# Kernel optimization log

Measured on AMD Instinct MI355X. Metric: run time of the kernel, lower is better.

## Reference

```python
import jax, jax.numpy as jnp
import numpy as np

RPN_BBOX_STD_DEV = np.array([0.1, 0.1, 0.2, 0.2], dtype=np.float32)
PRE_NMS_LIMIT = 6000
PROPOSAL_COUNT = 1000
NMS_THRESHOLD = 0.7
BATCH = 8
NUM_ANCHORS = 261888


def setup_inputs() -> dict:
    key = jax.random.key(0)
    k1, k2, k3, k4 = jax.random.split(key, 4)
    fg = jax.random.uniform(k1, (BATCH, NUM_ANCHORS), dtype=jnp.float32)
    rpn_probs = jnp.stack([1.0 - fg, fg], axis=-1)  # [B, N, 2] (bg, fg)
    rpn_bbox = jax.random.normal(k2, (BATCH, NUM_ANCHORS, 4), dtype=jnp.float32) * 0.5
    # valid normalized anchors: y_min < y_max, x_min < x_max, inside [0, 1]
    mins = jax.random.uniform(k3, (BATCH, NUM_ANCHORS, 2), minval=0.0, maxval=0.85)
    size = jax.random.uniform(k4, (BATCH, NUM_ANCHORS, 2), minval=0.02, maxval=0.15)
    anchors = jnp.concatenate([mins, mins + size], axis=-1)  # [B, N, 4]
    return {"rpn_probs": rpn_probs, "rpn_bbox": rpn_bbox, "anchors": anchors}


def apply_box_deltas(boxes, deltas):
    # boxes: [..., (y1, x1, y2, x2)], deltas: [..., (dy, dx, log(dh), log(dw))]
    h = boxes[..., 2] - boxes[..., 0]
    w = boxes[..., 3] - boxes[..., 1]
    cy = boxes[..., 0] + 0.5 * h + deltas[..., 0] * h
    cx = boxes[..., 1] + 0.5 * w + deltas[..., 1] * w
    h = h * jnp.exp(deltas[..., 2])
    w = w * jnp.exp(deltas[..., 3])
    y1 = cy - 0.5 * h
    x1 = cx - 0.5 * w
    return jnp.stack([y1, x1, y1 + h, x1 + w], axis=-1)


def pairwise_iou(boxes):
    # boxes: [N, 4] -> iou [N, N]
    y1, x1, y2, x2 = boxes[:, 0], boxes[:, 1], boxes[:, 2], boxes[:, 3]
    area = (y2 - y1) * (x2 - x1)
    ih = jnp.maximum(jnp.minimum(y2[:, None], y2[None, :]) - jnp.maximum(y1[:, None], y1[None, :]), 0.0)
    iw = jnp.maximum(jnp.minimum(x2[:, None], x2[None, :]) - jnp.maximum(x1[:, None], x1[None, :]), 0.0)
    inter = ih * iw
    union = area[:, None] + area[None, :] - inter
    return jnp.where(union > 0.0, inter / union, 0.0)


def nms_single(boxes):
    # boxes: [K, 4], already sorted by score descending (top_k sorted=True).
    # Greedy NMS: a box is suppressed if it overlaps (IoU > thresh) a kept,
    # higher-scoring box. Sequential suppression via lax.scan over rows.
    K = boxes.shape[0]
    iou = pairwise_iou(boxes)  # [K, K]
    order = jnp.arange(K)

    def step(keep, i):
        suppress = keep[i] & (iou[i] > NMS_THRESHOLD) & (order > i)
        return keep & ~suppress, None

    keep, _ = jax.lax.scan(step, jnp.ones((K,), dtype=bool), order)
    # gather kept boxes in score order, pad with zeros to PROPOSAL_COUNT
    rank = jnp.cumsum(keep) - 1
    valid = keep & (rank < PROPOSAL_COUNT)
    dest = jnp.where(valid, rank, PROPOSAL_COUNT)  # invalid rows -> scratch row
    out = jnp.zeros((PROPOSAL_COUNT + 1, 4), boxes.dtype).at[dest].set(boxes)
    return out[:PROPOSAL_COUNT]


def reference(rpn_probs, rpn_bbox, anchors):
    scores = rpn_probs[:, :, 1]  # fg prob [B, N]
    deltas = rpn_bbox * jnp.asarray(RPN_BBOX_STD_DEV).reshape(1, 1, 4)
    k = min(PRE_NMS_LIMIT, anchors.shape[1])
    top_scores, idx = jax.lax.top_k(scores, k)  # sorted descending, [B, K]
    deltas_k = jnp.take_along_axis(deltas, idx[..., None], axis=1)   # [B, K, 4]
    anchors_k = jnp.take_along_axis(anchors, idx[..., None], axis=1)  # [B, K, 4]
    boxes = jnp.clip(apply_box_deltas(anchors_k, deltas_k), 0.0, 1.0)
    proposals = jax.vmap(nms_single)(boxes)  # [B, PROPOSAL_COUNT, 4]
    return proposals
```

## Files before the change

kernel.cpp:

```cpp
#include <hip/hip_runtime.h>
#include <hip/hip_bf16.h>

typedef unsigned long long ull;

constexpr int BATCH = 8;
constexpr int NA    = 261888;
constexpr int KSEL  = 6000;
constexpr int PROP  = 1000;
constexpr int CAP   = 8192;
constexpr int NBINS = 8192;
constexpr int HB    = 16;
constexpr int NB    = (KSEL + 63) / 64;
constexpr int NWP   = 94;
constexpr int NBLK  = 94;
constexpr int NBLK2 = 47;

constexpr size_t OFF_CNT   = 0;
constexpr size_t OFF_TSEL  = 512;
constexpr size_t OFF_BOXES = 544;
constexpr size_t OFF_MASK  = 769024;
constexpr size_t OFF_DIAG  = OFF_MASK + 36096000;
constexpr size_t OFF_SUP   = OFF_DIAG + 385024;
constexpr size_t OFF_KEYS  = OFF_MASK;
constexpr size_t OFF_RANK  = OFF_MASK + 524288;
constexpr size_t OFF_HIST  = OFF_MASK + 2097152;

__device__ __forceinline__ int score_bin(float s) {
  int b = (int)(s * (float)NBINS);
  if (b < 0) b = 0;
  if (b > NBINS - 1) b = NBINS - 1;
  return b;
}

__global__ __launch_bounds__(256) void hist_kernel(const float2* __restrict__ probs,
                                                   unsigned int* __restrict__ hist) {
  __shared__ unsigned int lh[NBINS];
  for (int i = threadIdx.x; i < NBINS; i += 256) lh[i] = 0u;
  __syncthreads();
  int b = blockIdx.y;
  const float2* p = probs + (size_t)b * NA;
  for (int a = blockIdx.x * 256 + threadIdx.x; a < NA; a += HB * 256) {
    atomicAdd(&lh[score_bin(p[a].y)], 1u);
  }
  __syncthreads();
  unsigned int* gh = hist + ((size_t)b * HB + blockIdx.x) * NBINS;
  for (int i = threadIdx.x; i < NBINS; i += 256) gh[i] = lh[i];
}

__global__ __launch_bounds__(256) void thresh_kernel(const unsigned int* __restrict__ hist,
                                                     int* __restrict__ tsel) {
  constexpr int GR = NBINS / 256;
  __shared__ unsigned int ch[NBINS];
  __shared__ unsigned int gsum[256];
  int b = blockIdx.x;
  const unsigned int* h = hist + (size_t)b * HB * NBINS;
  for (int bin = threadIdx.x; bin < NBINS; bin += 256) {
    unsigned int s = 0;
    for (int k = 0; k < HB; ++k) s += h[(size_t)k * NBINS + bin];
    ch[bin] = s;
  }
  __syncthreads();
  unsigned int s = 0;
  int g0 = threadIdx.x * GR;
  for (int i = 0; i < GR; ++i) s += ch[g0 + i];
  gsum[threadIdx.x] = s;
  __syncthreads();
  if (threadIdx.x == 0) {
    unsigned int acc = 0;
    int g = 255;
    for (; g > 0; --g) {
      if (acc + gsum[g] >= (unsigned)KSEL) break;
      acc += gsum[g];
    }
    int t = g * GR;
    for (int bin = g * GR + GR - 1; bin >= g * GR; --bin) {
      acc += ch[bin];
      if (acc >= (unsigned)KSEL) { t = bin; break; }
    }
    tsel[b] = t;
  }
}

__global__ __launch_bounds__(256) void compact_kernel(const float2* __restrict__ probs,
                                                      const int* __restrict__ tsel,
                                                      int* __restrict__ cnt,
                                                      ull* __restrict__ keys) {
  __shared__ int lcnt, lbase;
  __shared__ ull lbuf[2048];
  int b = blockIdx.y;
  int t = tsel[b];
  if (threadIdx.x == 0) lcnt = 0;
  __syncthreads();
  const float2* p = probs + (size_t)b * NA;
  for (int a = blockIdx.x * blockDim.x + threadIdx.x; a < NA; a += gridDim.x * blockDim.x) {
    float s = p[a].y;
    if (score_bin(s) >= t) {
      int pos = atomicAdd(&lcnt, 1);
      unsigned int ib = ~__float_as_uint(s);
      lbuf[pos] = ((ull)ib << 32) | (unsigned int)a;
    }
  }
  __syncthreads();
  if (threadIdx.x == 0) lbase = atomicAdd(&cnt[b * 16], lcnt);
  __syncthreads();
  int n = lcnt, base = lbase;
  ull* kb = keys + (size_t)b * CAP;
  for (int i = threadIdx.x; i < n; i += 256) {
    int pos = base + i;
    if (pos < CAP) kb[pos] = lbuf[i];
  }
}

__global__ __launch_bounds__(256) void rank_kernel(const int* __restrict__ cnt,
                                                   const ull* __restrict__ keys,
                                                   unsigned int* __restrict__ rank) {
  int b = blockIdx.z;
  int n = cnt[b * 16];
  if (n > CAP) n = CAP;
  int i = blockIdx.x * 256 + threadIdx.x;
  if (i >= n) return;
  const ull* kb = keys + (size_t)b * CAP;
  ull my = kb[i];
  int n16 = (n + 15) & ~15;
  int nchunks = n16 >> 4;
  int hc = nchunks >> 1;
  int jlo = (blockIdx.y == 0) ? 0 : hc * 16;
  int jhi = (blockIdx.y == 0) ? hc * 16 : n16;
  unsigned int r = 0;
  for (int j = jlo; j < jhi; j += 16) {
#pragma unroll
    for (int t = 0; t < 16; ++t) {
      r += (kb[j + t] < my) ? 1u : 0u;
    }
  }
  if (r) atomicAdd(&rank[(size_t)b * CAP + i], r);
}

__global__ __launch_bounds__(256) void scatter_kernel(const float4* __restrict__ anchors4,
                                                      const float4* __restrict__ bbox4,
                                                      const int* __restrict__ cnt,
                                                      const ull* __restrict__ keys,
                                                      const unsigned int* __restrict__ rank,
                                                      float4* __restrict__ boxes4) {
#pragma clang fp contract(off)
  int b = blockIdx.y;
  int n = cnt[b * 16];
  if (n > CAP) n = CAP;
  int i = blockIdx.x * 256 + threadIdx.x;
  if (i >= n) return;
  unsigned int r = rank[(size_t)b * CAP + i];
  if (r >= (unsigned)KSEL) return;
  int a = (int)(unsigned int)(keys[(size_t)b * CAP + i] & 0xffffffffull);
  float4 anc = anchors4[(size_t)b * NA + a];
  float4 d   = bbox4[(size_t)b * NA + a];
  float h = anc.z - anc.x;
  float w = anc.w - anc.y;
  float dy = d.x * 0.1f, dx = d.y * 0.1f, dh = d.z * 0.2f, dw = d.w * 0.2f;
  float cy = (anc.x + (0.5f * h)) + (dy * h);
  float cx = (anc.y + (0.5f * w)) + (dx * w);
  float h2 = h * expf(dh);
  float w2 = w * expf(dw);
  float y1 = cy - 0.5f * h2;
  float x1 = cx - 0.5f * w2;
  float y2 = y1 + h2;
  float x2 = x1 + w2;
  y1 = fminf(fmaxf(y1, 0.f), 1.f);
  x1 = fminf(fmaxf(x1, 0.f), 1.f);
  y2 = fminf(fmaxf(y2, 0.f), 1.f);
  x2 = fminf(fmaxf(x2, 0.f), 1.f);
  boxes4[(size_t)b * KSEL + r] = make_float4(y1, x1, y2, x2);
}

__global__ __launch_bounds__(256) void mask_kernel(const float4* __restrict__ boxes4,
                                                   ull* __restrict__ mask,
                                                   ull* __restrict__ diagT,
                                                   ull* __restrict__ superT) {
  int cx = blockIdx.x, rb2 = blockIdx.y, b = blockIdx.z;
  int w0 = 2 * rb2;
  int cb0 = w0 + 4 * cx;
  if (cb0 >= NWP) return;
  __shared__ float4 colbox[4][64];
  __shared__ float  colca[4][64];
  __shared__ ull wtile[128][5];
  int tid = threadIdx.x, wv = tid >> 6, l = tid & 63;
  int cb = cb0 + wv;
  int rA = rb2 * 128 + l, rB = rA + 64;
  float4 zero = make_float4(0.f, 0.f, 0.f, 0.f);
  float4 boxA = (rA < KSEL) ? boxes4[(size_t)b * KSEL + rA] : zero;
  float4 boxB = (rB < KSEL) ? boxes4[(size_t)b * KSEL + rB] : zero;
  float areaA = (boxA.z - boxA.x) * (boxA.w - boxA.y);
  float areaB = (boxB.z - boxB.x) * (boxB.w - boxB.y);
  int c = cb * 64 + l;
  float4 cload = (cb < NB && c < KSEL) ? boxes4[(size_t)b * KSEL + c] : zero;
  colbox[wv][l] = cload;
  colca[wv][l] = (cload.z - cload.x) * (cload.w - cload.y);
  __syncthreads();
  ull bitsA = 0ull, bitsB = 0ull;
  if (cb < NB) {
#pragma unroll
    for (int u = 0; u < 64; ++u) {
      float4 cbx = colbox[wv][u];
      float ca = colca[wv][u];
      {
        float ih = fmaxf(fminf(boxA.z, cbx.z) - fmaxf(boxA.x, cbx.x), 0.f);
        float iw = fmaxf(fminf(boxA.w, cbx.w) - fmaxf(boxA.y, cbx.y), 0.f);
        float inter = ih * iw;
        float uni = (areaA + ca) - inter;
        float d = fmaf(-0.7f, uni, inter);
        float tt = 6e-7f * uni;
        bool keep;
        if (__builtin_fabsf(d) <= tt) keep = (inter / uni) > 0.7f;
        else keep = d > 0.f;
        if (keep) bitsA |= (1ull << u);
      }
      {
        float ih = fmaxf(fminf(boxB.z, cbx.z) - fmaxf(boxB.x, cbx.x), 0.f);
        float iw = fmaxf(fminf(boxB.w, cbx.w) - fmaxf(boxB.y, cbx.y), 0.f);
        float inter = ih * iw;
        float uni = (areaB + ca) - inter;
        float d = fmaf(-0.7f, uni, inter);
        float tt = 6e-7f * uni;
        bool keep;
        if (__builtin_fabsf(d) <= tt) keep = (inter / uni) > 0.7f;
        else keep = d > 0.f;
        if (keep) bitsB |= (1ull << u);
      }
    }
    if (cb == w0) {
      bitsA &= (l == 63) ? 0ull : (~0ull << (l + 1));
      diagT[((size_t)b * NBLK + w0) * 64 + l] = bitsA;
    }
    if (cb == w0 + 1) {
      superT[((size_t)b * NBLK + w0) * 64 + l] = bitsA;
      bitsB &= (l == 63) ? 0ull : (~0ull << (l + 1));
      diagT[((size_t)b * NBLK + w0 + 1) * 64 + l] = bitsB;
    }
    if (cb == w0 + 2) {
      superT[((size_t)b * NBLK + w0 + 1) * 64 + l] = bitsB;
    }
  }
  wtile[l][wv] = bitsA;
  wtile[l + 64][wv] = bitsB;
  __syncthreads();
  int base_row = rb2 * 128;
#pragma unroll
  for (int pass = 0; pass < 2; ++pass) {
    int idx = pass * 256 + tid;
    int rr = idx >> 2, w = idx & 3;
    int row = base_row + rr;
    if (row < KSEL && cb0 + w < NWP)
      mask[((size_t)b * KSEL + row) * NWP + cb0 + w] = wtile[rr][w];
  }
}

__global__ __launch_bounds__(64) void transq_kernel(ull* __restrict__ diagT) {
  __shared__ ull rows[64];
  int n = blockIdx.x, b = blockIdx.y;
  int l = threadIdx.x;
  ull* base = diagT + ((size_t)b * NBLK + n) * 64;
  rows[l] = base[l];
  __syncthreads();
  ull col = 0ull;
#pragma unroll
  for (int r = 0; r < 64; ++r)
    col |= ((rows[r] >> l) & 1ull) << r;
  base[l] = col;
}

__global__ __launch_bounds__(256, 1) void scan_kernel(const float4* __restrict__ boxes4,
                                                      const ull* __restrict__ mask,
                                                      const ull* __restrict__ diagT,
                                                      const ull* __restrict__ superT,
                                                      float4* __restrict__ out4) {
  __shared__ ull ldiagT[NBLK * 64];
  __shared__ ull lsuper[NBLK * 64];
  __shared__ ull S[96];
  __shared__ ull S_urg;
  __shared__ int klist[2][64];
  __shared__ int skeep[1024];
  __shared__ int s_kept, s_done, s_klen[2];
  int b = blockIdx.x;
  int tid = threadIdx.x;
  int lane = tid & 63;
  const ull* mb = mask + (size_t)b * KSEL * NWP;

  const ull* dt = diagT + (size_t)b * NBLK * 64;
  const ull* st = superT + (size_t)b * NBLK * 64;
  for (int i = tid; i < NBLK * 64; i += 256) { ldiagT[i] = dt[i]; lsuper[i] = st[i]; }
  if (tid < 96) S[tid] = 0ull;
  if (tid == 0) { s_kept = 0; s_done = 0; s_klen[0] = 0; s_klen[1] = 0; S_urg = 0ull; }
  __syncthreads();

  for (int n = 0; n < NBLK; ++n) {
    if (tid < 64) {
      ull Sn = S[n] | S_urg;
      int i0 = n * 64;
      ull colT = ldiagT[i0 + lane];
      ull sd = lsuper[i0 + lane];
      int nval = KSEL - i0;
      ull valid = (nval >= 64) ? ~0ull : ((1ull << nval) - 1ull);
      ull A = ~Sn & valid;
      ull K = 0ull;
      int kept = s_kept;
      int done = 0;
      while (A) {
        int u = __builtin_ctzll(A);
        ++kept;
        K |= (1ull << u);
        if (kept >= PROP) { done = 1; break; }
        ull sup = __ballot(((colT >> u) & 1ull) != 0ull);
        A &= ~(sup | (1ull << u));
      }
      int klen = __builtin_popcountll(K);
      int kbase = kept - klen;
      if ((K >> lane) & 1ull) {
        int rank = __builtin_popcountll(K & ((1ull << lane) - 1ull));
        skeep[kbase + rank] = i0 + lane;
        klist[n & 1][rank] = i0 + lane;
      }
      int klp = (klen + 7) & ~7;
      if (klen > 0 && lane >= klen && lane < klp)
        klist[n & 1][lane] = i0 + __builtin_ctzll(K);
      unsigned ulo = (unsigned)sd, uhi = (unsigned)(sd >> 32);
      if (!((K >> lane) & 1ull)) { ulo = 0u; uhi = 0u; }
#pragma unroll
      for (int m = 1; m < 64; m <<= 1) {
        ulo |= (unsigned)__shfl_xor((int)ulo, m, 64);
        uhi |= (unsigned)__shfl_xor((int)uhi, m, 64);
      }
      if (lane == 0) {
        s_klen[n & 1] = klen;
        S_urg = (ull)ulo | ((ull)uhi << 32);
        s_kept = kept;
        if (done || n == NBLK - 1) s_done = 1;
      }
    } else {
      int prev = (n & 1) ^ 1;
      int kl = s_klen[prev];
      int w = n + 1 + (tid - 64);
      if (kl > 0 && w < NB) {
        const int* kp = klist[prev];
        ull acc = 0ull;
        int klp = (kl + 7) & ~7;
        for (int ri = 0; ri < klp; ri += 8) {
#pragma unroll
          for (int t2 = 0; t2 < 8; ++t2)
            acc |= mb[(size_t)kp[ri + t2] * NWP + w];
        }
        S[w] |= acc;
      }
    }
    __syncthreads();
    if (s_done) break;
  }

  int fin = s_kept;
  if (fin > PROP) fin = PROP;
  for (int r2 = tid; r2 < PROP; r2 += 256) {
    float4 v = make_float4(0.f, 0.f, 0.f, 0.f);
    if (r2 < fin) v = boxes4[(size_t)b * KSEL + skeep[r2]];
    out4[(size_t)b * PROP + r2] = v;
  }
}

extern "C" void kernel_launch(void* const* d_in, const int* in_sizes, int n_in,
                              void* d_out, int out_size, void* d_ws, size_t ws_size,
                              hipStream_t stream) {
  const float2* probs   = (const float2*)d_in[0];
  const float4* bbox4   = (const float4*)d_in[1];
  const float4* anchors4= (const float4*)d_in[2];
  float4* out4 = (float4*)d_out;
  char* ws = (char*)d_ws;

  int* cnt           = (int*)(ws + OFF_CNT);
  int* tsel          = (int*)(ws + OFF_TSEL);
  float4* boxes4     = (float4*)(ws + OFF_BOXES);
  ull* maskw         = (ull*)(ws + OFF_MASK);
  ull* diagT         = (ull*)(ws + OFF_DIAG);
  ull* superT        = (ull*)(ws + OFF_SUP);
  ull* keys          = (ull*)(ws + OFF_KEYS);
  unsigned int* rank = (unsigned int*)(ws + OFF_RANK);
  unsigned int* hist = (unsigned int*)(ws + OFF_HIST);

  hipMemsetAsync(ws + OFF_CNT, 0, 544, stream);
  hipMemsetAsync(ws + OFF_KEYS, 0xFF, 524288, stream);
  hipMemsetAsync(ws + OFF_RANK, 0, 262144, stream);

  hipLaunchKernelGGL(hist_kernel,    dim3(HB, BATCH),      dim3(256), 0, stream, probs, hist);
  hipLaunchKernelGGL(thresh_kernel,  dim3(BATCH),          dim3(256), 0, stream, hist, tsel);
  hipLaunchKernelGGL(compact_kernel, dim3(128, BATCH),     dim3(256), 0, stream, probs, tsel, cnt, keys);
  hipLaunchKernelGGL(rank_kernel,    dim3(32, 2, BATCH),   dim3(256), 0, stream, cnt, keys, rank);
  hipLaunchKernelGGL(scatter_kernel, dim3(32, BATCH),      dim3(256), 0, stream, anchors4, bbox4, cnt, keys, rank, boxes4);
  hipLaunchKernelGGL(mask_kernel,    dim3(24, NBLK2, BATCH), dim3(256), 0, stream, boxes4, maskw, diagT, superT);
  hipLaunchKernelGGL(transq_kernel,  dim3(NBLK, BATCH),    dim3(64),  0, stream, diagT);
  hipLaunchKernelGGL(scan_kernel,    dim3(BATCH),          dim3(256), 0, stream, boxes4, maskw, diagT, superT, out4);
}
```

Measured before the change: 345.4 us.

## Process four row boxes per thread in NMS mask kernel with prescaled area threshold

The IoU mask kernel now gives each thread four row boxes instead of two, so every column box loaded from shared memory is reused across more rows and the row-block grid shrinks from 47 to 24. The IoU>0.7 test is rewritten algebraically as inter > (area_a+area_b)*0.7/1.7 using prescaled areas, with an exact division fallback near the threshold. Bits are packed in 16-bit chunks. Diagonal and superdiagonal block extraction is reworked for the wider tile, and the scan guards the last superdiagonal read. The cost is higher register pressure from four boxes plus the accumulators, which may lower occupancy.

After: 390.8 us. 13.1% more time.

```diff
diff --git a/kernel.cpp b/kernel.cpp
--- a/kernel.cpp
+++ b/kernel.cpp
@@ -13,7 +13,7 @@
 constexpr int NB    = (KSEL + 63) / 64;
 constexpr int NWP   = 94;
 constexpr int NBLK  = 94;
-constexpr int NBLK2 = 47;
+constexpr int NBLK4 = 24;
 
 constexpr size_t OFF_CNT   = 0;
 constexpr size_t OFF_TSEL  = 512;
@@ -175,76 +175,87 @@
                                                    ull* __restrict__ mask,
                                                    ull* __restrict__ diagT,
                                                    ull* __restrict__ superT) {
-  int cx = blockIdx.x, rb2 = blockIdx.y, b = blockIdx.z;
-  int w0 = 2 * rb2;
+#pragma clang fp contract(off)
+  constexpr float C717 = 0.4117647058823529f;
+  int cx = blockIdx.x, rb4 = blockIdx.y, b = blockIdx.z;
+  int w0 = 4 * rb4;
   int cb0 = w0 + 4 * cx;
   if (cb0 >= NWP) return;
   __shared__ float4 colbox[4][64];
-  __shared__ float  colca[4][64];
-  __shared__ ull wtile[128][5];
+  __shared__ float  colca7[4][64];
+  __shared__ float  colca [4][64];
+  __shared__ ull    wtile[256][5];
   int tid = threadIdx.x, wv = tid >> 6, l = tid & 63;
   int cb = cb0 + wv;
-  int rA = rb2 * 128 + l, rB = rA + 64;
+  int r0 = rb4 * 256 + l;
   float4 zero = make_float4(0.f, 0.f, 0.f, 0.f);
-  float4 boxA = (rA < KSEL) ? boxes4[(size_t)b * KSEL + rA] : zero;
-  float4 boxB = (rB < KSEL) ? boxes4[(size_t)b * KSEL + rB] : zero;
-  float areaA = (boxA.z - boxA.x) * (boxA.w - boxA.y);
-  float areaB = (boxB.z - boxB.x) * (boxB.w - boxB.y);
+  float4 boxR[4];
+  float  raF[4], ra7[4];
+#pragma unroll
+  for (int s = 0; s < 4; ++s) {
+    int r = r0 + 64 * s;
+    boxR[s] = (r < KSEL) ? boxes4[(size_t)b * KSEL + r] : zero;
+    raF[s] = (boxR[s].z - boxR[s].x) * (boxR[s].w - boxR[s].y);
+    ra7[s] = C717 * raF[s];
+  }
   int c = cb * 64 + l;
   float4 cload = (cb < NB && c < KSEL) ? boxes4[(size_t)b * KSEL + c] : zero;
+  float cav = (cload.z - cload.x) * (cload.w - cload.y);
   colbox[wv][l] = cload;
-  colca[wv][l] = (cload.z - cload.x) * (cload.w - cload.y);
-  __syncthreads();
-  ull bitsA = 0ull, bitsB = 0ull;
+  colca[wv][l]  = cav;
+  colca7[wv][l] = C717 * cav;
+  __syncthreads();
+  ull bits[4] = {0ull, 0ull, 0ull, 0ull};
   if (cb < NB) {
 #pragma unroll
-    for (int u = 0; u < 64; ++u) {
-      float4 cbx = colbox[wv][u];
-      float ca = colca[wv][u];
-      {
-        float ih = fmaxf(fminf(boxA.z, cbx.z) - fmaxf(boxA.x, cbx.x), 0.f);
-        float iw = fmaxf(fminf(boxA.w, cbx.w) - fmaxf(boxA.y, cbx.y), 0.f);
-        float inter = ih * iw;
-        float uni = (areaA + ca) - inter;
-        float d = fmaf(-0.7f, uni, inter);
-        float tt = 6e-7f * uni;
-        bool keep;
-        if (__builtin_fabsf(d) <= tt) keep = (inter / uni) > 0.7f;
-        else keep = d > 0.f;
-        if (keep) bitsA |= (1ull << u);
-      }
-      {
-        float ih = fmaxf(fminf(boxB.z, cbx.z) - fmaxf(boxB.x, cbx.x), 0.f);
-        float iw = fmaxf(fminf(boxB.w, cbx.w) - fmaxf(boxB.y, cbx.y), 0.f);
-        float inter = ih * iw;
-        float uni = (areaB + ca) - inter;
-        float d = fmaf(-0.7f, uni, inter);
-        float tt = 6e-7f * uni;
-        bool keep;
-        if (__builtin_fabsf(d) <= tt) keep = (inter / uni) > 0.7f;
-        else keep = d > 0.f;
-        if (keep) bitsB |= (1ull << u);
-      }
-    }
-    if (cb == w0) {
-      bitsA &= (l == 63) ? 0ull : (~0ull << (l + 1));
-      diagT[((size_t)b * NBLK + w0) * 64 + l] = bitsA;
-    }
-    if (cb == w0 + 1) {
-      superT[((size_t)b * NBLK + w0) * 64 + l] = bitsA;
-      bitsB &= (l == 63) ? 0ull : (~0ull << (l + 1));
-      diagT[((size_t)b * NBLK + w0 + 1) * 64 + l] = bitsB;
-    }
-    if (cb == w0 + 2) {
-      superT[((size_t)b * NBLK + w0 + 1) * 64 + l] = bitsB;
-    }
-  }
-  wtile[l][wv] = bitsA;
-  wtile[l + 64][wv] = bitsB;
-  __syncthreads();
-  int base_row = rb2 * 128;
-#pragma unroll
-  for (int pass = 0; pass < 2; ++pass) {
+    for (int g = 0; g < 4; ++g) {
+      unsigned chk[4] = {0u, 0u, 0u, 0u};
+#pragma unroll
+      for (int k = 0; k < 16; ++k) {
+        int u = g * 16 + k;
+        float4 cbx = colbox[wv][u];
+        float ca7 = colca7[wv][u];
+#pragma unroll
+        for (int s = 0; s < 4; ++s) {
+          float ih = fmaxf(fminf(boxR[s].z, cbx.z) - fmaxf(boxR[s].x, cbx.x), 0.f);
+          float iw = fmaxf(fminf(boxR[s].w, cbx.w) - fmaxf(boxR[s].y, cbx.y), 0.f);
+          float inter = ih * iw;
+          float t = ra7[s] + ca7;
+          float dd = inter - t;
+          float tt = 6e-7f * t;
+          bool keep;
+          if (__builtin_fabsf(dd) <= tt) {
+            float uni = (raF[s] + colca[wv][u]) - inter;
+            keep = (inter / uni) > 0.7f;
+          } else {
+            keep = dd > 0.f;
+          }
+          chk[s] |= (keep ? 1u : 0u) << k;
+        }
+      }
+#pragma unroll
+      for (int s = 0; s < 4; ++s) bits[s] |= (ull)chk[s] << (g * 16);
+    }
+    {
+      int sidx2 = 4 * cx + wv;
+      if (sidx2 < 4 && cb < NBLK) {
+        ull bm = bits[sidx2] & ((l == 63) ? 0ull : (~0ull << (l + 1)));
+        bits[sidx2] = bm;
+        diagT[((size_t)b * NBLK + cb) * 64 + l] = bm;
+      }
+      int sidx = 4 * cx + wv - 1;
+      if (sidx >= 0 && sidx < 4) {
+        int m = cb - 1;
+        superT[((size_t)b * NBLK + m) * 64 + l] = bits[sidx];
+      }
+    }
+  }
+#pragma unroll
+  for (int s = 0; s < 4; ++s) { wtile[l + 64 * s][wv] = bits[s]; }
+  __syncthreads();
+  int base_row = rb4 * 256;
+#pragma unroll
+  for (int pass = 0; pass < 4; ++pass) {
     int idx = pass * 256 + tid;
     int rr = idx >> 2, w = idx & 3;
     int row = base_row + rr;
@@ -296,7 +307,7 @@
       ull Sn = S[n] | S_urg;
       int i0 = n * 64;
       ull colT = ldiagT[i0 + lane];
-      ull sd = lsuper[i0 + lane];
+      ull sd = (n + 1 < NBLK) ? lsuper[i0 + lane] : 0ull;
       int nval = KSEL - i0;
       ull valid = (nval >= 64) ? ~0ull : ((1ull << nval) - 1ull);
       ull A = ~Sn & valid;
@@ -391,7 +402,7 @@
   hipLaunchKernelGGL(compact_kernel, dim3(128, BATCH),     dim3(256), 0, stream, probs, tsel, cnt, keys);
   hipLaunchKernelGGL(rank_kernel,    dim3(32, 2, BATCH),   dim3(256), 0, stream, cnt, keys, rank);
   hipLaunchKernelGGL(scatter_kernel, dim3(32, BATCH),      dim3(256), 0, stream, anchors4, bbox4, cnt, keys, rank, boxes4);
-  hipLaunchKernelGGL(mask_kernel,    dim3(24, NBLK2, BATCH), dim3(256), 0, stream, boxes4, maskw, diagT, superT);
+  hipLaunchKernelGGL(mask_kernel,    dim3(24, NBLK4, BATCH), dim3(256), 0, stream, boxes4, maskw, diagT, superT);
   hipLaunchKernelGGL(transq_kernel,  dim3(NBLK, BATCH),    dim3(64),  0, stream, diagT);
   hipLaunchKernelGGL(scan_kernel,    dim3(BATCH),          dim3(256), 0, stream, boxes4, maskw, diagT, superT, out4);
 }
```
